# Optimization experiments

Measured on AMD Instinct MI355X. Metric: run time of the kernel, lower is better.

## Reference

```python
import jax, jax.numpy as jnp
import numpy as np

B, L, D, E, H, TOP_K = 4, 2048, 1024, 8, 512, 2

def setup_inputs() -> dict:
    key = jax.random.key(0)
    k = jax.random.split(key, 6)
    x = jax.random.normal(k[0], (B, L, D), dtype=jnp.float32)
    gate_w = jax.random.normal(k[1], (D, E), dtype=jnp.float32) * 0.02
    gate_b = jnp.zeros((E,), jnp.float32)
    w1 = jax.random.normal(k[2], (E, D, H), dtype=jnp.float32) * 0.02
    b1 = jnp.zeros((E, H), jnp.float32)
    w2 = jax.random.normal(k[3], (E, H, D), dtype=jnp.float32) * 0.02
    b2 = jnp.zeros((E, D), jnp.float32)
    return {"x": x, "gate_w": gate_w, "gate_b": gate_b,
            "w1": w1, "b1": b1, "w2": w2, "b2": b2}

def reference(x, gate_w, gate_b, w1, b1, w2, b2):
    b, l, d = x.shape
    e = gate_w.shape[1]
    xf = x.reshape(-1, d)                      # [T, D], T = B*L
    t = xf.shape[0]
    # gating (eval mode: clean logits, no noise)
    logits = xf @ gate_w + gate_b              # [T, E]
    top_vals, top_idx = jax.lax.top_k(logits, TOP_K)
    top_gates = jax.nn.softmax(top_vals, axis=-1)
    gates = jnp.zeros((t, e), x.dtype).at[jnp.arange(t)[:, None], top_idx].set(top_gates)
    # per-expert 2-layer MLP computed densely, combined with sparse gates
    h = jax.nn.gelu(jnp.einsum('td,edh->eth', xf, w1) + b1[:, None, :], approximate=False)
    eo = jnp.einsum('eth,ehd->etd', h, w2) + b2[:, None, :]   # [E, T, D]
    out = jnp.einsum('te,etd->td', gates, eo)                 # weighted combine
    return out.reshape(b, l, d)
```

## Files before the change

### kernel.cpp

```cpp
#include <hip/hip_runtime.h>
#include <hip/hip_bf16.h>
#include <stdint.h>

#define B_    4
#define L_    2048
#define T_    8192
#define D_    1024
#define E_    8
#define H_    512

typedef __bf16  bf16x8 __attribute__((ext_vector_type(8)));
typedef float   f32x4  __attribute__((ext_vector_type(4)));
typedef unsigned short ushort_t;

__device__ __forceinline__ ushort_t f2bf(float f) {
    union { float f; unsigned u; } v; v.f = f;
    unsigned u = v.u;
    unsigned r = (u + 0x7fffu + ((u >> 16) & 1u)) >> 16;
    return (ushort_t)r;
}

__device__ __forceinline__ float gelu_fast(float v) {
    float x  = v * 0.70710678118654752f;
    float ax = fabsf(x);
    float t  = __builtin_amdgcn_rcpf(1.0f + 0.3275911f * ax);
    float y  = t * (0.254829592f +
               t * (-0.284496736f +
               t * (1.421413741f +
               t * (-1.453152027f +
               t * 1.061405429f))));
    float e  = __expf(-x * x);
    float er = 1.0f - y * e;
    er = copysignf(er, x);
    return 0.5f * v * (1.0f + er);
}

__device__ __forceinline__ void gld_lds16(const void* g, void* l) {
    __attribute__((address_space(3))) uint32_t* lp =
        reinterpret_cast<__attribute__((address_space(3))) uint32_t*>(
            reinterpret_cast<uintptr_t>(l));
    const __attribute__((address_space(1))) uint32_t* gp =
        reinterpret_cast<const __attribute__((address_space(1))) uint32_t*>(
            reinterpret_cast<uintptr_t>(g));
    __builtin_amdgcn_global_load_lds(gp, lp, 16, 0, 0);
}

__global__ __launch_bounds__(256) void prep_kernel(
    const float* __restrict__ w1, const float* __restrict__ w2,
    ushort_t* __restrict__ o1, ushort_t* __restrict__ o2,
    const float* __restrict__ x, const float* __restrict__ gw,
    const float* __restrict__ gb,
    int* __restrict__ eidx, float* __restrict__ gsel, ushort_t* __restrict__ xbf)
{
    __shared__ float smem[E_ * D_];
    const int bid = blockIdx.x;
    const int tid = threadIdx.x;

    if (bid < 8192) {
        float (*tile)[33] = reinterpret_cast<float(*)[33]>(smem);
        const int mz = bid >> 9;
        const int bxy = bid & 511;
        const float* src; ushort_t* dst; int C, R, sh;
        if (mz < E_) {
            src = w1 + (size_t)mz * D_ * H_; dst = o1 + (size_t)mz * D_ * H_;
            R = D_; C = H_; sh = 4;
        } else {
            const int m = mz - E_;
            src = w2 + (size_t)m * D_ * H_;  dst = o2 + (size_t)m * D_ * H_;
            R = H_; C = D_; sh = 5;
        }
        const int bx = bxy & ((1 << sh) - 1);
        const int by = bxy >> sh;
        const int r0 = by * 32, c0 = bx * 32;
        const int lr = tid >> 3;
        const int lc = (tid & 7) * 4;
        float4 v = *(const float4*)(src + (size_t)(r0 + lr) * C + c0 + lc);
        tile[lr][lc+0] = v.x; tile[lr][lc+1] = v.y;
        tile[lr][lc+2] = v.z; tile[lr][lc+3] = v.w;
        __syncthreads();
        ushort4 o;
        o.x = f2bf(tile[lc+0][lr]);
        o.y = f2bf(tile[lc+1][lr]);
        o.z = f2bf(tile[lc+2][lr]);
        o.w = f2bf(tile[lc+3][lr]);
        *(ushort4*)(dst + (size_t)(c0 + lr) * R + r0 + lc) = o;
        return;
    }

    float (*gwT)[D_] = reinterpret_cast<float(*)[D_]>(smem);
    const int gbid = bid - 8192;

    #pragma unroll
    for (int it = 0; it < 8; ++it) {
        const int idx = it * 256 + tid;
        float4 v = *(const float4*)(gw + (size_t)idx * 4);
        const int row = idx >> 1;
        const int col = (idx & 1) * 4;
        gwT[col+0][row] = v.x;
        gwT[col+1][row] = v.y;
        gwT[col+2][row] = v.z;
        gwT[col+3][row] = v.w;
    }
    __syncthreads();

    const int wave = tid >> 6;
    const int lane = tid & 63;

    #pragma unroll
    for (int it = 0; it < 2; ++it) {
        const int t = gbid * 8 + wave * 2 + it;
        const float* xr = x + (size_t)t * D_;
        ushort_t* xbr = xbf + (size_t)t * D_;

        float acc[E_];
        #pragma unroll
        for (int e = 0; e < E_; ++e) acc[e] = 0.f;

        #pragma unroll
        for (int j = 0; j < 4; ++j) {
            const int d = j * 256 + lane * 4;
            float4 xv = *(const float4*)(xr + d);
            ushort4 o;
            o.x = f2bf(xv.x); o.y = f2bf(xv.y); o.z = f2bf(xv.z); o.w = f2bf(xv.w);
            *(ushort4*)(xbr + d) = o;
            #pragma unroll
            for (int e = 0; e < E_; ++e) {
                float4 w = *(const float4*)(&gwT[e][d]);
                acc[e] += xv.x * w.x + xv.y * w.y + xv.z * w.z + xv.w * w.w;
            }
        }
        #pragma unroll
        for (int s = 1; s < 64; s <<= 1) {
            #pragma unroll
            for (int e = 0; e < E_; ++e)
                acc[e] += __shfl_xor(acc[e], s, 64);
        }
        if (lane == 0) {
            float v[E_];
            #pragma unroll
            for (int e = 0; e < E_; ++e) v[e] = acc[e] + gb[e];
            int i0 = 0;
            #pragma unroll
            for (int e = 1; e < E_; ++e) if (v[e] > v[i0]) i0 = e;
            int i1 = (i0 == 0) ? 1 : 0;
            #pragma unroll
            for (int e = 0; e < E_; ++e) if (e != i0 && v[e] > v[i1]) i1 = e;
            float g0 = 1.f / (1.f + expf(v[i1] - v[i0]));
            eidx[t] = i0 | (i1 << 8);
            gsel[t] = g0;
        }
    }
}

__global__ __launch_bounds__(256) void bucket_kernel(
    const int* __restrict__ eidx, const float* __restrict__ gsel,
    int* __restrict__ counts, int* __restrict__ btok, float* __restrict__ bgate,
    uint32_t* __restrict__ tpos)
{
    __shared__ int lcnt[E_];
    __shared__ int lbase[E_];
    const int tid = threadIdx.x;
    if (tid < E_) lcnt[tid] = 0;
    __syncthreads();
    const int t = blockIdx.x * 256 + tid;
    const int pk = eidx[t];
    const float g0 = gsel[t];
    const int i0 = pk & 0xff, i1 = (pk >> 8) & 0xff;
    const int p0 = atomicAdd(&lcnt[i0], 1);
    const int p1 = atomicAdd(&lcnt[i1], 1);
    __syncthreads();
    if (tid < E_) lbase[tid] = atomicAdd(&counts[tid], lcnt[tid]);
    __syncthreads();
    const int q0 = lbase[i0] + p0, q1 = lbase[i1] + p1;
    btok[i0 * T_ + q0] = t; bgate[i0 * T_ + q0] = g0;
    btok[i1 * T_ + q1] = t; bgate[i1 * T_ + q1] = 1.f - g0;
    tpos[t] = (uint32_t)((i0 << 13) | q0) | ((uint32_t)((i1 << 13) | q1) << 16);
}

__global__ __launch_bounds__(256) void mlp1_kernel(
    const ushort_t* __restrict__ xbf, const ushort_t* __restrict__ w1t,
    const float* __restrict__ b1,
    const int* __restrict__ counts,
    const int* __restrict__ btok, ushort_t* __restrict__ hbuf)
{
    const int e   = blockIdx.z;
    const int n_e = counts[e];
    const int m0  = blockIdx.x * 64;
    if (m0 >= n_e) return;
    int off = 0;
    for (int i = 0; i < e; ++i) off += counts[i];
    const int n0  = blockIdx.y * 64;

    __shared__ ushort_t As[2][64 * 64];
    __shared__ ushort_t Bs[2][64 * 64];

    const int tid  = threadIdx.x;
    const int lane = tid & 63;
    const int wave = tid >> 6;

    const int srow = tid >> 3;
    const int cg   = (tid & 7) ^ (srow & 7);

    const ushort_t* aptr[2];
    #pragma unroll
    for (int i = 0; i < 2; ++i) {
        int m = m0 + i * 32 + srow;
        int tok = btok[e * T_ + (m < n_e ? m : n_e - 1)];
        aptr[i] = xbf + (size_t)tok * D_ + cg * 8;
    }
    const ushort_t* w1e = w1t + (size_t)e * (H_ * D_);
    const ushort_t* bptr[2];
    #pragma unroll
    for (int i = 0; i < 2; ++i)
        bptr[i] = w1e + (size_t)(n0 + i * 32 + srow) * D_ + cg * 8;

    const int fm   = lane & 15;
    const int quad = lane >> 4;
    const int wm   = (wave & 1) * 32;
    const int wn   = (wave >> 1) * 32;

    f32x4 acc[2][2];
    #pragma unroll
    for (int i = 0; i < 2; ++i)
        #pragma unroll
        for (int j = 0; j < 2; ++j)
            { acc[i][j][0]=0.f; acc[i][j][1]=0.f; acc[i][j][2]=0.f; acc[i][j][3]=0.f; }

    #define STAGE1(bufi, koff)                                              \
        do {                                                                \
            char* al_ = (char*)(&As[bufi][0]) + (wave << 10);               \
            char* bl_ = (char*)(&Bs[bufi][0]) + (wave << 10);               \
            _Pragma("unroll")                                               \
            for (int i_ = 0; i_ < 2; ++i_)                                  \
                gld_lds16(aptr[i_] + (koff), al_ + (i_ << 12));             \
            _Pragma("unroll")                                               \
            for (int i_ = 0; i_ < 2; ++i_)                                  \
                gld_lds16(bptr[i_] + (koff), bl_ + (i_ << 12));             \
        } while (0)

    STAGE1(0, 0);
    __builtin_amdgcn_sched_barrier(0);
    STAGE1(1, 64);
    __builtin_amdgcn_sched_barrier(0);

    int buf = 0;
    for (int k0 = 0; k0 < D_; k0 += 64) {
        if (k0 + 64 < D_) asm volatile("s_waitcnt vmcnt(4)" ::: "memory");
        else              asm volatile("s_waitcnt vmcnt(0)" ::: "memory");
        __builtin_amdgcn_s_barrier();
        const char* Ab = (const char*)(&As[buf][0]);
        const char* Bb = (const char*)(&Bs[buf][0]);
        #pragma unroll
        for (int kk = 0; kk < 2; ++kk) {
            const int grp = kk * 4 + quad;
            bf16x8 af[2], bfr[2];
            #pragma unroll
            for (int i = 0; i < 2; ++i) {
                int ra = wm + i * 16 + fm;
                af[i]  = *(const bf16x8*)(Ab + ra * 128 + ((grp ^ (ra & 7)) << 4));
            }
            #pragma unroll
            for (int j = 0; j < 2; ++j) {
                int rb = wn + j * 16 + fm;
                bfr[j] = *(const bf16x8*)(Bb + rb * 128 + ((grp ^ (rb & 7)) << 4));
            }
            #pragma unroll
            for (int i = 0; i < 2; ++i)
                #pragma unroll
                for (int j = 0; j < 2; ++j)
                    acc[i][j] = __builtin_amdgcn_mfma_f32_16x16x32_bf16(af[i], bfr[j], acc[i][j], 0, 0, 0);
        }
        if (k0 + 128 < D_) {
            asm volatile("s_waitcnt lgkmcnt(0)" ::: "memory");
            __builtin_amdgcn_s_barrier();
            STAGE1(buf, k0 + 128);
            __builtin_amdgcn_sched_barrier(0);
        }
        buf ^= 1;
    }
    #undef STAGE1

    float bcol[2];
    #pragma unroll
    for (int j = 0; j < 2; ++j)
        bcol[j] = b1[e * H_ + n0 + wn + j * 16 + fm];
    #pragma unroll
    for (int i = 0; i < 2; ++i) {
        #pragma unroll
        for (int r = 0; r < 4; ++r) {
            int m = m0 + wm + i * 16 + quad * 4 + r;
            if (m >= n_e) continue;
            ushort_t* hrow = hbuf + (size_t)(off + m) * H_ + n0;
            #pragma unroll
            for (int j = 0; j < 2; ++j)
                hrow[wn + j * 16 + fm] = f2bf(gelu_fast(acc[i][j][r] + bcol[j]));
        }
    }
}

__global__ __launch_bounds__(256) void mlp2_kernel(
    const ushort_t* __restrict__ hbuf, const ushort_t* __restrict__ w2t,
    const float* __restrict__ b2,
    const int* __restrict__ counts,
    const float* __restrict__ bgate, ushort_t* __restrict__ obuf)
{
    const int e   = blockIdx.z;
    const int n_e = counts[e];
    const int m0  = blockIdx.x * 64;
    if (m0 >= n_e) return;
    int off = 0;
    for (int i = 0; i < e; ++i) off += counts[i];
    const int n0  = blockIdx.y * 64;

    __shared__ ushort_t As[2][64 * 64];
    __shared__ ushort_t Bs[2][64 * 64];

    const int tid  = threadIdx.x;
    const int lane = tid & 63;
    const int wave = tid >> 6;

    const int srow = tid >> 3;
    const int cg   = (tid & 7) ^ (srow & 7);

    const ushort_t* aptr[2];
    #pragma unroll
    for (int i = 0; i < 2; ++i)
        aptr[i] = hbuf + (size_t)(off + m0 + i * 32 + srow) * H_ + cg * 8;
    const ushort_t* w2e = w2t + (size_t)e * (D_ * H_);
    const ushort_t* bptr[2];
    #pragma unroll
    for (int i = 0; i < 2; ++i)
        bptr[i] = w2e + (size_t)(n0 + i * 32 + srow) * H_ + cg * 8;

    const int fm   = lane & 15;
    const int quad = lane >> 4;
    const int wm   = (wave & 1) * 32;
    const int wn   = (wave >> 1) * 32;

    f32x4 acc[2][2];
    #pragma unroll
    for (int i = 0; i < 2; ++i)
        #pragma unroll
        for (int j = 0; j < 2; ++j)
            { acc[i][j][0]=0.f; acc[i][j][1]=0.f; acc[i][j][2]=0.f; acc[i][j][3]=0.f; }

    #define STAGE2(bufi, koff)                                              \
        do {                                                                \
            char* al_ = (char*)(&As[bufi][0]) + (wave << 10);               \
            char* bl_ = (char*)(&Bs[bufi][0]) + (wave << 10);               \
            _Pragma("unroll")                                               \
            for (int i_ = 0; i_ < 2; ++i_)                                  \
                gld_lds16(aptr[i_] + (koff), al_ + (i_ << 12));             \
            _Pragma("unroll")                                               \
            for (int i_ = 0; i_ < 2; ++i_)                                  \
                gld_lds16(bptr[i_] + (koff), bl_ + (i_ << 12));             \
        } while (0)

    STAGE2(0, 0);
    __builtin_amdgcn_sched_barrier(0);
    STAGE2(1, 64);
    __builtin_amdgcn_sched_barrier(0);

    int buf = 0;
    for (int k0 = 0; k0 < H_; k0 += 64) {
        if (k0 + 64 < H_) asm volatile("s_waitcnt vmcnt(4)" ::: "memory");
        else              asm volatile("s_waitcnt vmcnt(0)" ::: "memory");
        __builtin_amdgcn_s_barrier();
        const char* Ab = (const char*)(&As[buf][0]);
        const char* Bb = (const char*)(&Bs[buf][0]);
        #pragma unroll
        for (int kk = 0; kk < 2; ++kk) {
            const int grp = kk * 4 + quad;
            bf16x8 af[2], bfr[2];
            #pragma unroll
            for (int i = 0; i < 2; ++i) {
                int ra = wm + i * 16 + fm;
                af[i]  = *(const bf16x8*)(Ab + ra * 128 + ((grp ^ (ra & 7)) << 4));
            }
            #pragma unroll
            for (int j = 0; j < 2; ++j) {
                int rb = wn + j * 16 + fm;
                bfr[j] = *(const bf16x8*)(Bb + rb * 128 + ((grp ^ (rb & 7)) << 4));
            }
            #pragma unroll
            for (int i = 0; i < 2; ++i)
                #pragma unroll
                for (int j = 0; j < 2; ++j)
                    acc[i][j] = __builtin_amdgcn_mfma_f32_16x16x32_bf16(af[i], bfr[j], acc[i][j], 0, 0, 0);
        }
        if (k0 + 128 < H_) {
            asm volatile("s_waitcnt lgkmcnt(0)" ::: "memory");
            __builtin_amdgcn_s_barrier();
            STAGE2(buf, k0 + 128);
            __builtin_amdgcn_sched_barrier(0);
        }
        buf ^= 1;
    }
    #undef STAGE2

    float bcol[2];
    #pragma unroll
    for (int j = 0; j < 2; ++j)
        bcol[j] = b2[e * D_ + n0 + wn + j * 16 + fm];
    #pragma unroll
    for (int i = 0; i < 2; ++i) {
        #pragma unroll
        for (int r = 0; r < 4; ++r) {
            int m = m0 + wm + i * 16 + quad * 4 + r;
            if (m >= n_e) continue;
            float g = bgate[e * T_ + m];
            ushort_t* orow = obuf + (size_t)(off + m) * D_ + n0;
            #pragma unroll
            for (int j = 0; j < 2; ++j)
                orow[wn + j * 16 + fm] = f2bf((acc[i][j][r] + bcol[j]) * g);
        }
    }
}

__global__ __launch_bounds__(256) void combine_kernel(
    const ushort_t* __restrict__ obuf, const uint32_t* __restrict__ tpos,
    const int* __restrict__ counts, float* __restrict__ out)
{
    const int tid = threadIdx.x;
    const int t = blockIdx.x * 2 + (tid >> 7);
    const int c = (tid & 127) * 8;
    const uint32_t pk = tpos[t];
    const int e0 = (pk >> 13) & 7, p0 = pk & 0x1fff;
    const int e1 = (pk >> 29) & 7, p1 = (pk >> 16) & 0x1fff;

    const int4 ca = *(const int4*)(counts);
    const int4 cb = *(const int4*)(counts + 4);
    int pre[8];
    pre[0] = 0;
    pre[1] = ca.x;
    pre[2] = pre[1] + ca.y;
    pre[3] = pre[2] + ca.z;
    pre[4] = pre[3] + ca.w;
    pre[5] = pre[4] + cb.x;
    pre[6] = pre[5] + cb.y;
    pre[7] = pre[6] + cb.z;
    int off0 = 0, off1 = 0;
    #pragma unroll
    for (int i = 1; i < 8; ++i) {
        off0 = (e0 == i) ? pre[i] : off0;
        off1 = (e1 == i) ? pre[i] : off1;
    }

    const size_t s0 = (size_t)(off0 + p0) * D_ + c;
    const size_t s1 = (size_t)(off1 + p1) * D_ + c;
    bf16x8 a = *(const bf16x8*)(obuf + s0);
    bf16x8 b = *(const bf16x8*)(obuf + s1);
    float4 o0, o1;
    o0.x = (float)a[0] + (float)b[0];
    o0.y = (float)a[1] + (float)b[1];
    o0.z = (float)a[2] + (float)b[2];
    o0.w = (float)a[3] + (float)b[3];
    o1.x = (float)a[4] + (float)b[4];
    o1.y = (float)a[5] + (float)b[5];
    o1.z = (float)a[6] + (float)b[6];
    o1.w = (float)a[7] + (float)b[7];
    float* orow = out + (size_t)t * D_ + c;
    *(float4*)(orow)     = o0;
    *(float4*)(orow + 4) = o1;
}

extern "C" void kernel_launch(void* const* d_in, const int* in_sizes, int n_in,
                              void* d_out, int out_size, void* d_ws, size_t ws_size,
                              hipStream_t stream)
{
    const float* x  = (const float*)d_in[0];
    const float* gw = (const float*)d_in[1];
    const float* gb = (const float*)d_in[2];
    const float* w1 = (const float*)d_in[3];
    const float* b1 = (const float*)d_in[4];
    const float* w2 = (const float*)d_in[5];
    const float* b2 = (const float*)d_in[6];
    float* out = (float*)d_out;

    char* ws = (char*)d_ws;
    int*   counts  = (int*)ws;
    int*   btok    = (int*)(ws + 256);
    float* bgate   = (float*)(ws + 256 + (size_t)E_*T_*4);
    size_t p = 256 + 2ull * E_ * T_ * 4;
    int*      eidx = (int*)(ws + p);      p += (size_t)T_ * 4;
    float*    gsel = (float*)(ws + p);    p += (size_t)T_ * 4;
    uint32_t* tpos = (uint32_t*)(ws + p); p += (size_t)T_ * 4;
    ushort_t* xbf  = (ushort_t*)(ws + p); p += (size_t)T_*D_*2;
    ushort_t* w1t  = (ushort_t*)(ws + p); p += (size_t)E_*H_*D_*2;
    ushort_t* w2t  = (ushort_t*)(ws + p); p += (size_t)E_*D_*H_*2;
    ushort_t* hbuf = (ushort_t*)(ws + p); p += ((size_t)2*T_+128)*H_*2;
    ushort_t* obuf = (ushort_t*)(ws + p);

    (void)hipMemsetAsync(counts, 0, 64, stream);

    prep_kernel<<<8192 + T_/8, 256, 0, stream>>>(
        w1, w2, w1t, w2t, x, gw, gb, eidx, gsel, xbf);
    bucket_kernel<<<T_/256, 256, 0, stream>>>(eidx, gsel, counts, btok, bgate, tpos);
    mlp1_kernel<<<dim3(T_/64, H_/64, E_), 256, 0, stream>>>(
        xbf, w1t, b1, counts, btok, hbuf);
    mlp2_kernel<<<dim3(T_/64, D_/64, E_), 256, 0, stream>>>(
        hbuf, w2t, b2, counts, bgate, obuf);
    combine_kernel<<<T_/2, 256, 0, stream>>>(obuf, tpos, counts, out);
}
```

Before: 215.9 us.

## Fuse expert MLP layers into one kernel keeping hidden activations in LDS

Merges the two per-expert GEMM kernels into one. Each block handles 32 routed tokens of one expert: it computes the full 512-wide GELU hidden tile into shared memory, then runs the second GEMM from LDS. This is meant to remove the global round trip of the hidden buffer and one kernel launch. The cost is lower per-block parallelism: blocks shrink to 32 rows, and each one now reads the whole expert weight matrices, so W1 and W2 traffic per token grows.

```diff
diff --git a/kernel.cpp b/kernel.cpp
--- a/kernel.cpp
+++ b/kernel.cpp
@@ -177,244 +177,200 @@
     tpos[t] = (uint32_t)((i0 << 13) | q0) | ((uint32_t)((i1 << 13) | q1) << 16);
 }
 
-__global__ __launch_bounds__(256) void mlp1_kernel(
+__global__ __launch_bounds__(256) void mlp_fused(
     const ushort_t* __restrict__ xbf, const ushort_t* __restrict__ w1t,
-    const float* __restrict__ b1,
-    const int* __restrict__ counts,
-    const int* __restrict__ btok, ushort_t* __restrict__ hbuf)
+    const float* __restrict__ b1, const ushort_t* __restrict__ w2t,
+    const float* __restrict__ b2, const int* __restrict__ counts,
+    const int* __restrict__ btok, const float* __restrict__ bgate,
+    ushort_t* __restrict__ obuf)
 {
-    const int e   = blockIdx.z;
+    const int e  = blockIdx.x & 7;
+    const int mb = blockIdx.x >> 3;
     const int n_e = counts[e];
-    const int m0  = blockIdx.x * 64;
+    const int m0 = mb * 32;
     if (m0 >= n_e) return;
     int off = 0;
     for (int i = 0; i < e; ++i) off += counts[i];
-    const int n0  = blockIdx.y * 64;
-
-    __shared__ ushort_t As[2][64 * 64];
-    __shared__ ushort_t Bs[2][64 * 64];
+
+    __shared__ ushort_t As[2][32 * 64];
+    __shared__ ushort_t Ws[2][128 * 64];
+    __shared__ ushort_t Hs[32 * 512];
 
     const int tid  = threadIdx.x;
     const int lane = tid & 63;
     const int wave = tid >> 6;
-
     const int srow = tid >> 3;
     const int cg   = (tid & 7) ^ (srow & 7);
-
-    const ushort_t* aptr[2];
-    #pragma unroll
-    for (int i = 0; i < 2; ++i) {
-        int m = m0 + i * 32 + srow;
-        int tok = btok[e * T_ + (m < n_e ? m : n_e - 1)];
-        aptr[i] = xbf + (size_t)tok * D_ + cg * 8;
-    }
-    const ushort_t* w1e = w1t + (size_t)e * (H_ * D_);
-    const ushort_t* bptr[2];
-    #pragma unroll
-    for (int i = 0; i < 2; ++i)
-        bptr[i] = w1e + (size_t)(n0 + i * 32 + srow) * D_ + cg * 8;
-
     const int fm   = lane & 15;
     const int quad = lane >> 4;
-    const int wm   = (wave & 1) * 32;
-    const int wn   = (wave >> 1) * 32;
-
-    f32x4 acc[2][2];
-    #pragma unroll
-    for (int i = 0; i < 2; ++i)
-        #pragma unroll
-        for (int j = 0; j < 2; ++j)
-            { acc[i][j][0]=0.f; acc[i][j][1]=0.f; acc[i][j][2]=0.f; acc[i][j][3]=0.f; }
-
-    #define STAGE1(bufi, koff)                                              \
+
+    const int gm   = m0 + srow;
+    const int tokr = btok[e * T_ + (gm < n_e ? gm : n_e - 1)];
+    const ushort_t* aptr = xbf + (size_t)tokr * D_ + cg * 8;
+    const ushort_t* w1e = w1t + (size_t)e * (H_ * D_);
+    const ushort_t* w2e = w2t + (size_t)e * (D_ * H_);
+
+    #define STAGEP1(bufi, koff)                                             \
         do {                                                                \
             char* al_ = (char*)(&As[bufi][0]) + (wave << 10);               \
-            char* bl_ = (char*)(&Bs[bufi][0]) + (wave << 10);               \
+            char* bl_ = (char*)(&Ws[bufi][0]) + (wave << 10);               \
+            gld_lds16(aptr + (koff), al_);                                  \
             _Pragma("unroll")                                               \
-            for (int i_ = 0; i_ < 2; ++i_)                                  \
-                gld_lds16(aptr[i_] + (koff), al_ + (i_ << 12));             \
-            _Pragma("unroll")                                               \
-            for (int i_ = 0; i_ < 2; ++i_)                                  \
+            for (int i_ = 0; i_ < 4; ++i_)                                  \
                 gld_lds16(bptr[i_] + (koff), bl_ + (i_ << 12));             \
         } while (0)
 
-    STAGE1(0, 0);
-    __builtin_amdgcn_sched_barrier(0);
-    STAGE1(1, 64);
-    __builtin_amdgcn_sched_barrier(0);
-
-    int buf = 0;
-    for (int k0 = 0; k0 < D_; k0 += 64) {
-        if (k0 + 64 < D_) asm volatile("s_waitcnt vmcnt(4)" ::: "memory");
-        else              asm volatile("s_waitcnt vmcnt(0)" ::: "memory");
-        __builtin_amdgcn_s_barrier();
-        const char* Ab = (const char*)(&As[buf][0]);
-        const char* Bb = (const char*)(&Bs[buf][0]);
-        #pragma unroll
-        for (int kk = 0; kk < 2; ++kk) {
-            const int grp = kk * 4 + quad;
-            bf16x8 af[2], bfr[2];
-            #pragma unroll
-            for (int i = 0; i < 2; ++i) {
-                int ra = wm + i * 16 + fm;
-                af[i]  = *(const bf16x8*)(Ab + ra * 128 + ((grp ^ (ra & 7)) << 4));
-            }
-            #pragma unroll
-            for (int j = 0; j < 2; ++j) {
-                int rb = wn + j * 16 + fm;
-                bfr[j] = *(const bf16x8*)(Bb + rb * 128 + ((grp ^ (rb & 7)) << 4));
-            }
+    #define STAGEP2(bufi, koff)                                             \
+        do {                                                                \
+            char* bl_ = (char*)(&Ws[bufi][0]) + (wave << 10);               \
+            _Pragma("unroll")                                               \
+            for (int i_ = 0; i_ < 4; ++i_)                                  \
+                gld_lds16(a2ptr[i_] + (koff), bl_ + (i_ << 12));            \
+        } while (0)
+
+    const int wn1 = wave * 32;
+    for (int p = 0; p < 4; ++p) {
+        const int n0 = p * 128;
+        const ushort_t* bptr[4];
+        #pragma unroll
+        for (int i = 0; i < 4; ++i)
+            bptr[i] = w1e + (size_t)(n0 + i * 32 + srow) * D_ + cg * 8;
+
+        f32x4 acc[2][2];
+        #pragma unroll
+        for (int i = 0; i < 2; ++i)
+            #pragma unroll
+            for (int j = 0; j < 2; ++j)
+                { acc[i][j][0]=0.f; acc[i][j][1]=0.f; acc[i][j][2]=0.f; acc[i][j][3]=0.f; }
+
+        __syncthreads();
+        STAGEP1(0, 0);
+        STAGEP1(1, 64);
+        __builtin_amdgcn_sched_barrier(0);
+
+        int buf = 0;
+        for (int k0 = 0; k0 < D_; k0 += 64) {
+            if (k0 + 64 < D_) asm volatile("s_waitcnt vmcnt(5)" ::: "memory");
+            else              asm volatile("s_waitcnt vmcnt(0)" ::: "memory");
+            __builtin_amdgcn_s_barrier();
+            const char* Ab = (const char*)(&As[buf][0]);
+            const char* Bb = (const char*)(&Ws[buf][0]);
+            #pragma unroll
+            for (int kk = 0; kk < 2; ++kk) {
+                const int grp = kk * 4 + quad;
+                bf16x8 af[2], bfr[2];
+                #pragma unroll
+                for (int i = 0; i < 2; ++i) {
+                    int ra = i * 16 + fm;
+                    af[i]  = *(const bf16x8*)(Ab + ra * 128 + ((grp ^ (ra & 7)) << 4));
+                }
+                #pragma unroll
+                for (int j = 0; j < 2; ++j) {
+                    int rb = wn1 + j * 16 + fm;
+                    bfr[j] = *(const bf16x8*)(Bb + rb * 128 + ((grp ^ (rb & 7)) << 4));
+                }
+                #pragma unroll
+                for (int i = 0; i < 2; ++i)
+                    #pragma unroll
+                    for (int j = 0; j < 2; ++j)
+                        acc[i][j] = __builtin_amdgcn_mfma_f32_16x16x32_bf16(af[i], bfr[j], acc[i][j], 0, 0, 0);
+            }
+            if (k0 + 128 < D_) {
+                asm volatile("s_waitcnt lgkmcnt(0)" ::: "memory");
+                __builtin_amdgcn_s_barrier();
+                STAGEP1(buf, k0 + 128);
+                __builtin_amdgcn_sched_barrier(0);
+            }
+            buf ^= 1;
+        }
+
+        #pragma unroll
+        for (int j = 0; j < 2; ++j) {
+            const int hcol = n0 + wn1 + j * 16 + fm;
+            const float b1v = b1[e * H_ + hcol];
+            const int gidx = hcol >> 3;
             #pragma unroll
             for (int i = 0; i < 2; ++i)
                 #pragma unroll
-                for (int j = 0; j < 2; ++j)
-                    acc[i][j] = __builtin_amdgcn_mfma_f32_16x16x32_bf16(af[i], bfr[j], acc[i][j], 0, 0, 0);
-        }
-        if (k0 + 128 < D_) {
-            asm volatile("s_waitcnt lgkmcnt(0)" ::: "memory");
+                for (int r = 0; r < 4; ++r) {
+                    const int m = i * 16 + quad * 4 + r;
+                    char* hp = (char*)Hs + m * 1024 + ((gidx ^ (m & 7)) << 4) + (hcol & 7) * 2;
+                    *(ushort_t*)hp = f2bf(gelu_fast(acc[i][j][r] + b1v));
+                }
+        }
+    }
+
+    const int wm2  = (wave & 1) * 64;
+    const int wn2  = (wave >> 1) * 16;
+    const int tcol = wn2 + fm;
+    const int mrow = m0 + tcol;
+    const bool valid = mrow < n_e;
+    const float g = bgate[e * T_ + (valid ? mrow : 0)];
+    ushort_t* orow = obuf + (size_t)(off + (valid ? mrow : 0)) * D_;
+
+    for (int mp = 0; mp < 8; ++mp) {
+        const int d0 = mp * 128;
+        const ushort_t* a2ptr[4];
+        #pragma unroll
+        for (int i = 0; i < 4; ++i)
+            a2ptr[i] = w2e + (size_t)(d0 + i * 32 + srow) * H_ + cg * 8;
+
+        f32x4 acc2[4];
+        #pragma unroll
+        for (int i = 0; i < 4; ++i)
+            { acc2[i][0]=0.f; acc2[i][1]=0.f; acc2[i][2]=0.f; acc2[i][3]=0.f; }
+
+        __syncthreads();
+        STAGEP2(0, 0);
+        STAGEP2(1, 64);
+        __builtin_amdgcn_sched_barrier(0);
+
+        int buf = 0;
+        for (int k0 = 0; k0 < H_; k0 += 64) {
+            if (k0 + 64 < H_) asm volatile("s_waitcnt vmcnt(4)" ::: "memory");
+            else              asm volatile("s_waitcnt vmcnt(0)" ::: "memory");
             __builtin_amdgcn_s_barrier();
-            STAGE1(buf, k0 + 128);
-            __builtin_amdgcn_sched_barrier(0);
-        }
-        buf ^= 1;
-    }
-    #undef STAGE1
-
-    float bcol[2];
-    #pragma unroll
-    for (int j = 0; j < 2; ++j)
-        bcol[j] = b1[e * H_ + n0 + wn + j * 16 + fm];
-    #pragma unroll
-    for (int i = 0; i < 2; ++i) {
-        #pragma unroll
-        for (int r = 0; r < 4; ++r) {
-            int m = m0 + wm + i * 16 + quad * 4 + r;
-            if (m >= n_e) continue;
-            ushort_t* hrow = hbuf + (size_t)(off + m) * H_ + n0;
-            #pragma unroll
-            for (int j = 0; j < 2; ++j)
-                hrow[wn + j * 16 + fm] = f2bf(gelu_fast(acc[i][j][r] + bcol[j]));
-        }
-    }
-}
-
-__global__ __launch_bounds__(256) void mlp2_kernel(
-    const ushort_t* __restrict__ hbuf, const ushort_t* __restrict__ w2t,
-    const float* __restrict__ b2,
-    const int* __restrict__ counts,
-    const float* __restrict__ bgate, ushort_t* __restrict__ obuf)
-{
-    const int e   = blockIdx.z;
-    const int n_e = counts[e];
-    const int m0  = blockIdx.x * 64;
-    if (m0 >= n_e) return;
-    int off = 0;
-    for (int i = 0; i < e; ++i) off += counts[i];
-    const int n0  = blockIdx.y * 64;
-
-    __shared__ ushort_t As[2][64 * 64];
-    __shared__ ushort_t Bs[2][64 * 64];
-
-    const int tid  = threadIdx.x;
-    const int lane = tid & 63;
-    const int wave = tid >> 6;
-
-    const int srow = tid >> 3;
-    const int cg   = (tid & 7) ^ (srow & 7);
-
-    const ushort_t* aptr[2];
-    #pragma unroll
-    for (int i = 0; i < 2; ++i)
-        aptr[i] = hbuf + (size_t)(off + m0 + i * 32 + srow) * H_ + cg * 8;
-    const ushort_t* w2e = w2t + (size_t)e * (D_ * H_);
-    const ushort_t* bptr[2];
-    #pragma unroll
-    for (int i = 0; i < 2; ++i)
-        bptr[i] = w2e + (size_t)(n0 + i * 32 + srow) * H_ + cg * 8;
-
-    const int fm   = lane & 15;
-    const int quad = lane >> 4;
-    const int wm   = (wave & 1) * 32;
-    const int wn   = (wave >> 1) * 32;
-
-    f32x4 acc[2][2];
-    #pragma unroll
-    for (int i = 0; i < 2; ++i)
-        #pragma unroll
-        for (int j = 0; j < 2; ++j)
-            { acc[i][j][0]=0.f; acc[i][j][1]=0.f; acc[i][j][2]=0.f; acc[i][j][3]=0.f; }
-
-    #define STAGE2(bufi, koff)                                              \
-        do {                                                                \
-            char* al_ = (char*)(&As[bufi][0]) + (wave << 10);               \
-            char* bl_ = (char*)(&Bs[bufi][0]) + (wave << 10);               \
-            _Pragma("unroll")                                               \
-            for (int i_ = 0; i_ < 2; ++i_)                                  \
-                gld_lds16(aptr[i_] + (koff), al_ + (i_ << 12));             \
-            _Pragma("unroll")                                               \
-            for (int i_ = 0; i_ < 2; ++i_)                                  \
-                gld_lds16(bptr[i_] + (koff), bl_ + (i_ << 12));             \
-        } while (0)
-
-    STAGE2(0, 0);
-    __builtin_amdgcn_sched_barrier(0);
-    STAGE2(1, 64);
-    __builtin_amdgcn_sched_barrier(0);
-
-    int buf = 0;
-    for (int k0 = 0; k0 < H_; k0 += 64) {
-        if (k0 + 64 < H_) asm volatile("s_waitcnt vmcnt(4)" ::: "memory");
-        else              asm volatile("s_waitcnt vmcnt(0)" ::: "memory");
-        __builtin_amdgcn_s_barrier();
-        const char* Ab = (const char*)(&As[buf][0]);
-        const char* Bb = (const char*)(&Bs[buf][0]);
-        #pragma unroll
-        for (int kk = 0; kk < 2; ++kk) {
-            const int grp = kk * 4 + quad;
-            bf16x8 af[2], bfr[2];
-            #pragma unroll
-            for (int i = 0; i < 2; ++i) {
-                int ra = wm + i * 16 + fm;
-                af[i]  = *(const bf16x8*)(Ab + ra * 128 + ((grp ^ (ra & 7)) << 4));
-            }
-            #pragma unroll
-            for (int j = 0; j < 2; ++j) {
-                int rb = wn + j * 16 + fm;
-                bfr[j] = *(const bf16x8*)(Bb + rb * 128 + ((grp ^ (rb & 7)) << 4));
-            }
-            #pragma unroll
-            for (int i = 0; i < 2; ++i)
-                #pragma unroll
-                for (int j = 0; j < 2; ++j)
-                    acc[i][j] = __builtin_amdgcn_mfma_f32_16x16x32_bf16(af[i], bfr[j], acc[i][j], 0, 0, 0);
-        }
-        if (k0 + 128 < H_) {
-            asm volatile("s_waitcnt lgkmcnt(0)" ::: "memory");
-            __builtin_amdgcn_s_barrier();
-            STAGE2(buf, k0 + 128);
-            __builtin_amdgcn_sched_barrier(0);
-        }
-        buf ^= 1;
-    }
-    #undef STAGE2
-
-    float bcol[2];
-    #pragma unroll
-    for (int j = 0; j < 2; ++j)
-        bcol[j] = b2[e * D_ + n0 + wn + j * 16 + fm];
-    #pragma unroll
-    for (int i = 0; i < 2; ++i) {
-        #pragma unroll
-        for (int r = 0; r < 4; ++r) {
-            int m = m0 + wm + i * 16 + quad * 4 + r;
-            if (m >= n_e) continue;
-            float g = bgate[e * T_ + m];
-            ushort_t* orow = obuf + (size_t)(off + m) * D_ + n0;
-            #pragma unroll
-            for (int j = 0; j < 2; ++j)
-                orow[wn + j * 16 + fm] = f2bf((acc[i][j][r] + bcol[j]) * g);
-        }
-    }
+            const char* Wb = (const char*)(&Ws[buf][0]);
+            #pragma unroll
+            for (int kk = 0; kk < 2; ++kk) {
+                const int grp = kk * 4 + quad;
+                const int kg  = (k0 >> 3) + grp;
+                bf16x8 af2[4];
+                bf16x8 bh = *(const bf16x8*)((const char*)Hs + tcol * 1024 + ((kg ^ (tcol & 7)) << 4));
+                #pragma unroll
+                for (int i = 0; i < 4; ++i) {
+                    int ra = wm2 + i * 16 + fm;
+                    af2[i] = *(const bf16x8*)(Wb + ra * 128 + ((grp ^ (ra & 7)) << 4));
+                }
+                #pragma unroll
+                for (int i = 0; i < 4; ++i)
+                    acc2[i] = __builtin_amdgcn_mfma_f32_16x16x32_bf16(af2[i], bh, acc2[i], 0, 0, 0);
+            }
+            if (k0 + 128 < H_) {
+                asm volatile("s_waitcnt lgkmcnt(0)" ::: "memory");
+                __builtin_amdgcn_s_barrier();
+                STAGEP2(buf, k0 + 128);
+                __builtin_amdgcn_sched_barrier(0);
+            }
+            buf ^= 1;
+        }
+
+        if (valid) {
+            #pragma unroll
+            for (int i = 0; i < 4; ++i) {
+                const int db = d0 + wm2 + i * 16 + quad * 4;
+                const float4 bb = *(const float4*)(b2 + e * D_ + db);
+                ushort4 o;
+                o.x = f2bf((acc2[i][0] + bb.x) * g);
+                o.y = f2bf((acc2[i][1] + bb.y) * g);
+                o.z = f2bf((acc2[i][2] + bb.z) * g);
+                o.w = f2bf((acc2[i][3] + bb.w) * g);
+                *(ushort4*)(orow + db) = o;
+            }
+        }
+    }
+    #undef STAGEP1
+    #undef STAGEP2
 }
 
 __global__ __launch_bounds__(256) void combine_kernel(
@@ -488,7 +444,6 @@
     ushort_t* xbf  = (ushort_t*)(ws + p); p += (size_t)T_*D_*2;
     ushort_t* w1t  = (ushort_t*)(ws + p); p += (size_t)E_*H_*D_*2;
     ushort_t* w2t  = (ushort_t*)(ws + p); p += (size_t)E_*D_*H_*2;
-    ushort_t* hbuf = (ushort_t*)(ws + p); p += ((size_t)2*T_+128)*H_*2;
     ushort_t* obuf = (ushort_t*)(ws + p);
 
     (void)hipMemsetAsync(counts, 0, 64, stream);
@@ -496,9 +451,7 @@
     prep_kernel<<<8192 + T_/8, 256, 0, stream>>>(
         w1, w2, w1t, w2t, x, gw, gb, eidx, gsel, xbf);
     bucket_kernel<<<T_/256, 256, 0, stream>>>(eidx, gsel, counts, btok, bgate, tpos);
-    mlp1_kernel<<<dim3(T_/64, H_/64, E_), 256, 0, stream>>>(
-        xbf, w1t, b1, counts, btok, hbuf);
-    mlp2_kernel<<<dim3(T_/64, D_/64, E_), 256, 0, stream>>>(
-        hbuf, w2t, b2, counts, bgate, obuf);
+    mlp_fused<<<2048, 256, 0, stream>>>(
+        xbf, w1t, b1, w2t, b2, counts, btok, bgate, obuf);
     combine_kernel<<<T_/2, 256, 0, stream>>>(obuf, tpos, counts, out);
 }
```

Result: slower. 242.7 us (+12.4%).
